# Performance work log

Measured on AMD Instinct MI355X. Metric: run time of the kernel, lower is better.

## Reference

```python
import jax, jax.numpy as jnp
import numpy as np

L_K = 6  # number of nearest neighbors (matches module-level L_K)
N_POINTS = 4096


def setup_inputs() -> dict:
    key = jax.random.key(0)
    k1, k2, k3, k4 = jax.random.split(key, 4)
    input_t = jax.random.normal(k1, (1, 3, N_POINTS), dtype=jnp.float32)
    sf_t = jax.random.normal(k2, (1, 3, N_POINTS), dtype=jnp.float32) * 0.1
    y1 = jax.random.normal(k3, (1, 3, N_POINTS), dtype=jnp.float32)
    pred = jax.random.normal(k4, (1, 3, N_POINTS), dtype=jnp.float32)
    return {"input_t": input_t, "sf_t": sf_t, "y1": y1, "pred": pred}


def _kabsch(pc, recon):
    # Standard Kabsch rigid-transform estimation (pc, recon: [N,3]).
    cp = pc.mean(axis=0)
    cr = recon.mean(axis=0)
    H = (pc - cp).T @ (recon - cr)  # [3,3] cross-covariance
    U, S, Vt = jnp.linalg.svd(H)
    d = jnp.sign(jnp.linalg.det(Vt.T @ U.T))
    # R = V diag(1,1,d) U^T  (reflection fix)
    R = Vt.T @ (jnp.stack([jnp.float32(1.0), jnp.float32(1.0), d])[:, None] * U.T)
    t = cr - R @ cp
    return R, t


def _knn_laplace(centers, ref, k):
    # centers: [N,3] query points (x1); ref: [M,3] cloud to gather neighbors from.
    # Matches: squared_dist over all pairs, topk smallest along ref dim,
    # grouping gather, then Laplacian differencing normalized by (k-1).
    d2 = jnp.sum((centers[:, None, :] - ref[None, :, :]) ** 2, axis=-1)  # [N,M]
    _, idx = jax.lax.top_k(-d2, k)  # k smallest distances -> neighbor indices [N,k]
    grouped = ref[idx]  # [N,k,3] gather
    return jnp.sum(grouped - centers[:, None, :], axis=1) / float(k - 1)  # [N,3]


def reference(input_t, sf_t, y1, pred):
    # Rigid reconstruction: we use a single cluster covering all points
    # (deterministic stand-in for the CPU-side DBSCAN clustering), so the
    # whole cloud is rigidly reconstructed via Kabsch, then detached
    # (original code calls .detach() on the Kabsch reconstruction).
    pc = input_t[0].T        # [N,3]
    recon = pc + sf_t[0].T   # [N,3]
    R, t = _kabsch(pc, recon)
    rigid_recon = jax.lax.stop_gradient(pc @ R.T + t)  # [N,3]

    yT = y1[0].T  # [N,3]
    laplace_y = _knn_laplace(rigid_recon, yT, L_K)          # cross-cloud kNN Laplacian
    laplace_x = _knn_laplace(rigid_recon, rigid_recon, L_K)  # self kNN Laplacian
    laplace_reduced = laplace_x - laplace_y  # [N,3]

    # Single cluster = all points: subtract mean Laplacian difference.
    rigid_refine = rigid_recon - jnp.mean(laplace_reduced, axis=0)  # [N,3]

    # L1 loss (mean reduction) vs student prediction.
    return jnp.mean(jnp.abs(rigid_refine - pred[0].T))
```

## Files before the change

### kernel.cpp

```cpp
#include <hip/hip_runtime.h>
#include <math.h>

#define NP 4096
#define KNN 6
#define NCHUNK 16
#define CHUNK 256

typedef unsigned int u32;

__device__ inline double det3(const double M[3][3]) {
  return M[0][0]*(M[1][1]*M[2][2]-M[1][2]*M[2][1])
       - M[0][1]*(M[1][0]*M[2][2]-M[1][2]*M[2][0])
       + M[0][2]*(M[1][0]*M[2][1]-M[1][1]*M[2][0]);
}

__device__ inline double wave_reduce(double v) {
#pragma unroll
  for (int o = 32; o > 0; o >>= 1) v += __shfl_down(v, o);
  return v;
}

#define TOP6_INSERT(key)                                   \
  { u32 _t;                                                \
    _t = min(b0, key); key = max(b0, key); b0 = _t;        \
    _t = min(b1, key); key = max(b1, key); b1 = _t;        \
    _t = min(b2, key); key = max(b2, key); b2 = _t;        \
    _t = min(b3, key); key = max(b3, key); b3 = _t;        \
    _t = min(b4, key); key = max(b4, key); b4 = _t;        \
    _t = min(b5, key); key = max(b5, key); b5 = _t; }

__global__ __launch_bounds__(256) void k1_kabsch(const float* __restrict__ in,
                                                 const float* __restrict__ sf,
                                                 float* __restrict__ rx,
                                                 float* __restrict__ ry,
                                                 float* __restrict__ rz) {
  const int tid = threadIdx.x;
  const int lane = tid & 63, wv = tid >> 6;
  double acc[15];
#pragma unroll
  for (int q = 0; q < 15; ++q) acc[q] = 0.0;
  for (int i = tid; i < NP; i += 256) {
    double px = in[i], py = in[NP + i], pz = in[2*NP + i];
    double qx = px + (double)sf[i];
    double qy = py + (double)sf[NP + i];
    double qz = pz + (double)sf[2*NP + i];
    acc[0] += px; acc[1] += py; acc[2] += pz;
    acc[3] += qx; acc[4] += qy; acc[5] += qz;
    acc[6] += px*qx; acc[7]  += px*qy; acc[8]  += px*qz;
    acc[9] += py*qx; acc[10] += py*qy; acc[11] += py*qz;
    acc[12]+= pz*qx; acc[13] += pz*qy; acc[14] += pz*qz;
  }
  __shared__ double wred[4][15];
#pragma unroll
  for (int q = 0; q < 15; ++q) {
    double v = wave_reduce(acc[q]);
    if (lane == 0) wred[wv][q] = v;
  }
  __syncthreads();
  __shared__ float Rs[9];
  __shared__ float ts[3];
  if (tid == 0) {
    double tot[15];
    for (int q = 0; q < 15; ++q)
      tot[q] = wred[0][q] + wred[1][q] + wred[2][q] + wred[3][q];
    const double invN = 1.0 / (double)NP;
    double cp[3] = { tot[0]*invN, tot[1]*invN, tot[2]*invN };
    double cr[3] = { tot[3]*invN, tot[4]*invN, tot[5]*invN };
    double H[3][3];
    for (int a = 0; a < 3; ++a)
      for (int b = 0; b < 3; ++b)
        H[a][b] = tot[6 + a*3 + b] - (double)NP * cp[a] * cr[b];
    double A[3][3];
    for (int a = 0; a < 3; ++a)
      for (int b = 0; b < 3; ++b)
        A[a][b] = H[0][a]*H[0][b] + H[1][a]*H[1][b] + H[2][a]*H[2][b];
    double V[3][3] = {{1,0,0},{0,1,0},{0,0,1}};
    const int PQ[3][2] = {{0,1},{0,2},{1,2}};
    for (int sweep = 0; sweep < 12; ++sweep) {
      for (int r = 0; r < 3; ++r) {
        const int p = PQ[r][0], q = PQ[r][1];
        double apq = A[p][q];
        if (fabs(apq) > 1e-300) {
          double theta = (A[q][q] - A[p][p]) / (2.0 * apq);
          double tt = copysign(1.0, theta) / (fabs(theta) + sqrt(theta*theta + 1.0));
          double c = 1.0 / sqrt(tt*tt + 1.0);
          double s = tt * c;
          for (int k = 0; k < 3; ++k) { double akp=A[k][p], akq=A[k][q]; A[k][p]=c*akp - s*akq; A[k][q]=s*akp + c*akq; }
          for (int k = 0; k < 3; ++k) { double apk=A[p][k], aqk=A[q][k]; A[p][k]=c*apk - s*aqk; A[q][k]=s*apk + c*aqk; }
          for (int k = 0; k < 3; ++k) { double vkp=V[k][p], vkq=V[k][q]; V[k][p]=c*vkp - s*vkq; V[k][q]=s*vkp + c*vkq; }
        }
      }
    }
    int ord[3] = {0,1,2};
    for (int a = 0; a < 2; ++a)
      for (int b = a + 1; b < 3; ++b)
        if (A[ord[b]][ord[b]] > A[ord[a]][ord[a]]) { int t2 = ord[a]; ord[a] = ord[b]; ord[b] = t2; }
    double Vc[3][3], Uc[3][3];
    for (int j = 0; j < 3; ++j) {
      const int e = ord[j];
      double lam = A[e][e] > 0.0 ? A[e][e] : 0.0;
      double sv = sqrt(lam);
      double isv = sv > 0.0 ? 1.0 / sv : 0.0;
      for (int a = 0; a < 3; ++a) Vc[a][j] = V[a][e];
      for (int a = 0; a < 3; ++a)
        Uc[a][j] = (H[a][0]*Vc[0][j] + H[a][1]*Vc[1][j] + H[a][2]*Vc[2][j]) * isv;
    }
    double dd = (det3(Uc) * det3(Vc)) >= 0.0 ? 1.0 : -1.0;
    double R[3][3];
    for (int a = 0; a < 3; ++a)
      for (int b = 0; b < 3; ++b)
        R[a][b] = Vc[a][0]*Uc[b][0] + Vc[a][1]*Uc[b][1] + dd * Vc[a][2]*Uc[b][2];
    double tv[3];
    for (int a = 0; a < 3; ++a)
      tv[a] = cr[a] - (R[a][0]*cp[0] + R[a][1]*cp[1] + R[a][2]*cp[2]);
    for (int a = 0; a < 3; ++a) {
      Rs[a*3+0] = (float)R[a][0];
      Rs[a*3+1] = (float)R[a][1];
      Rs[a*3+2] = (float)R[a][2];
      ts[a] = (float)tv[a];
    }
  }
  __syncthreads();
  for (int i = tid; i < NP; i += 256) {
    float px = in[i], py = in[NP + i], pz = in[2*NP + i];
    rx[i] = Rs[0]*px + Rs[1]*py + Rs[2]*pz + ts[0];
    ry[i] = Rs[3]*px + Rs[4]*py + Rs[5]*pz + ts[1];
    rz[i] = Rs[6]*px + Rs[7]*py + Rs[8]*pz + ts[2];
  }
}

__global__ __launch_bounds__(256) void k2_partial(const float* __restrict__ rx,
                                                  const float* __restrict__ ry,
                                                  const float* __restrict__ rz,
                                                  const float* __restrict__ ycloud,
                                                  u32* __restrict__ part) {
  __shared__ float4 sc[CHUNK];
  const int tid = threadIdx.x;
  const int chunk = blockIdx.x;
  const int cblk  = blockIdx.y;
  const int cloud = blockIdx.z;
  const int j0 = chunk * CHUNK;
  if (cloud == 0) {
    sc[tid] = make_float4(rx[j0 + tid], ry[j0 + tid], rz[j0 + tid], 0.f);
  } else {
    sc[tid] = make_float4(ycloud[j0 + tid], ycloud[NP + j0 + tid],
                          ycloud[2*NP + j0 + tid], 0.f);
  }
  __syncthreads();
  const int ci = cblk * 256 + tid;
  const float cx = rx[ci], cy = ry[ci], cz = rz[ci];
  u32 b0 = ~0u, b1 = ~0u, b2 = ~0u, b3 = ~0u, b4 = ~0u, b5 = ~0u;
#pragma unroll 8
  for (int j = 0; j < CHUNK; ++j) {
    float4 c = sc[j];
    float dx = c.x - cx, dy = c.y - cy, dz = c.z - cz;
    float d2 = fmaf(dx, dx, fmaf(dy, dy, dz * dz));
    u32 key = (__float_as_uint(d2) & 0xFFFFF000u) | (u32)(j0 + j);
    TOP6_INSERT(key);
  }
  u32* o = part + (size_t)(cloud * NCHUNK + chunk) * KNN * NP + ci;
  o[0*NP] = b0; o[1*NP] = b1; o[2*NP] = b2;
  o[3*NP] = b3; o[4*NP] = b4; o[5*NP] = b5;
}

__global__ __launch_bounds__(256) void k2_merge(const u32* __restrict__ part,
                                                const float* __restrict__ rx,
                                                const float* __restrict__ ry,
                                                const float* __restrict__ rz,
                                                const float* __restrict__ ycloud,
                                                double* __restrict__ blockpart) {
  const int tid = threadIdx.x;
  const int lane = tid & 63, wv = tid >> 6;
  const int ci = blockIdx.x * 256 + tid;
  double d0, d1, d2s;
  {
    u32 b0 = ~0u, b1 = ~0u, b2 = ~0u, b3 = ~0u, b4 = ~0u, b5 = ~0u;
    for (int c = 0; c < NCHUNK; ++c) {
      const u32* p = part + (size_t)c * KNN * NP + ci;
#pragma unroll
      for (int e = 0; e < KNN; ++e) {
        u32 key = p[(size_t)e * NP];
        TOP6_INSERT(key);
      }
    }
    u32 bk[KNN] = { b0, b1, b2, b3, b4, b5 };
    float s0 = 0.f, s1 = 0.f, s2 = 0.f;
#pragma unroll
    for (int k = 0; k < KNN; ++k) {
      int idx = (int)(bk[k] & 0xFFFu);
      s0 += rx[idx]; s1 += ry[idx]; s2 += rz[idx];
    }
    d0 = s0; d1 = s1; d2s = s2;
  }
  {
    u32 b0 = ~0u, b1 = ~0u, b2 = ~0u, b3 = ~0u, b4 = ~0u, b5 = ~0u;
    for (int c = 0; c < NCHUNK; ++c) {
      const u32* p = part + (size_t)(NCHUNK + c) * KNN * NP + ci;
#pragma unroll
      for (int e = 0; e < KNN; ++e) {
        u32 key = p[(size_t)e * NP];
        TOP6_INSERT(key);
      }
    }
    u32 bk[KNN] = { b0, b1, b2, b3, b4, b5 };
    float s0 = 0.f, s1 = 0.f, s2 = 0.f;
#pragma unroll
    for (int k = 0; k < KNN; ++k) {
      int idx = (int)(bk[k] & 0xFFFu);
      s0 += ycloud[idx]; s1 += ycloud[NP + idx]; s2 += ycloud[2*NP + idx];
    }
    d0 -= s0; d1 -= s1; d2s -= s2;
  }
  __shared__ double wred[4][3];
  double v0 = wave_reduce(d0), v1 = wave_reduce(d1), v2 = wave_reduce(d2s);
  if (lane == 0) { wred[wv][0] = v0; wred[wv][1] = v1; wred[wv][2] = v2; }
  __syncthreads();
  if (tid == 0) {
    blockpart[blockIdx.x * 3 + 0] = wred[0][0] + wred[1][0] + wred[2][0] + wred[3][0];
    blockpart[blockIdx.x * 3 + 1] = wred[0][1] + wred[1][1] + wred[2][1] + wred[3][1];
    blockpart[blockIdx.x * 3 + 2] = wred[0][2] + wred[1][2] + wred[2][2] + wred[3][2];
  }
}

__global__ __launch_bounds__(256) void k3_final(const double* __restrict__ blockpart,
                                                const float* __restrict__ rx,
                                                const float* __restrict__ ry,
                                                const float* __restrict__ rz,
                                                const float* __restrict__ pred,
                                                float* __restrict__ out) {
  const int tid = threadIdx.x;
  const int lane = tid & 63, wv = tid >> 6;
  __shared__ float m[3];
  if (tid == 0) {
    double s0 = 0.0, s1 = 0.0, s2 = 0.0;
    for (int b = 0; b < 16; ++b) {
      s0 += blockpart[b*3 + 0];
      s1 += blockpart[b*3 + 1];
      s2 += blockpart[b*3 + 2];
    }
    const double sc = 0.2 / (double)NP;
    m[0] = (float)(s0 * sc); m[1] = (float)(s1 * sc); m[2] = (float)(s2 * sc);
  }
  __syncthreads();
  const float m0 = m[0], m1 = m[1], m2 = m[2];
  double s = 0.0;
  for (int i = tid; i < NP; i += 256) {
    s += (double)fabsf(rx[i] - m0 - pred[i]);
    s += (double)fabsf(ry[i] - m1 - pred[NP + i]);
    s += (double)fabsf(rz[i] - m2 - pred[2*NP + i]);
  }
  __shared__ double wred[4];
  double v = wave_reduce(s);
  if (lane == 0) wred[wv] = v;
  __syncthreads();
  if (tid == 0)
    out[0] = (float)((wred[0] + wred[1] + wred[2] + wred[3]) / (3.0 * (double)NP));
}

extern "C" void kernel_launch(void* const* d_in, const int* in_sizes, int n_in,
                              void* d_out, int out_size, void* d_ws, size_t ws_size,
                              hipStream_t stream) {
  const float* in   = (const float*)d_in[0];
  const float* sf   = (const float*)d_in[1];
  const float* y1   = (const float*)d_in[2];
  const float* pred = (const float*)d_in[3];

  u32* part = (u32*)d_ws;
  double* blockpart = (double*)(part + (size_t)2 * NCHUNK * KNN * NP);
  float* rx = (float*)(blockpart + 48);
  float* ry = rx + NP;
  float* rz = ry + NP;

  k1_kabsch<<<1, 256, 0, stream>>>(in, sf, rx, ry, rz);
  k2_partial<<<dim3(NCHUNK, 16, 2), 256, 0, stream>>>(rx, ry, rz, y1, part);
  k2_merge<<<16, 256, 0, stream>>>(part, rx, ry, rz, y1, blockpart);
  k3_final<<<1, 256, 0, stream>>>(blockpart, rx, ry, rz, pred, (float*)d_out);
}
```

Measured before the change: 69.03 us.

## Fuse transform into kNN scan, merge final reduction, use float Jacobi

```diff
diff --git a/kernel.cpp b/kernel.cpp
--- a/kernel.cpp
+++ b/kernel.cpp
@@ -7,33 +7,30 @@
 #define CHUNK 256
 
 typedef unsigned int u32;
-
-__device__ inline double det3(const double M[3][3]) {
+typedef unsigned long long u64;
+
+__device__ inline double wave_reduce(double v) {
+#pragma unroll
+  for (int o = 32; o > 0; o >>= 1) v += __shfl_down(v, o);
+  return v;
+}
+
+__device__ inline float det3f(const float M[3][3]) {
   return M[0][0]*(M[1][1]*M[2][2]-M[1][2]*M[2][1])
        - M[0][1]*(M[1][0]*M[2][2]-M[1][2]*M[2][0])
        + M[0][2]*(M[1][0]*M[2][1]-M[1][1]*M[2][0]);
 }
 
-__device__ inline double wave_reduce(double v) {
-#pragma unroll
-  for (int o = 32; o > 0; o >>= 1) v += __shfl_down(v, o);
-  return v;
-}
-
-#define TOP6_INSERT(key)                                   \
-  { u32 _t;                                                \
-    _t = min(b0, key); key = max(b0, key); b0 = _t;        \
-    _t = min(b1, key); key = max(b1, key); b1 = _t;        \
-    _t = min(b2, key); key = max(b2, key); b2 = _t;        \
-    _t = min(b3, key); key = max(b3, key); b3 = _t;        \
-    _t = min(b4, key); key = max(b4, key); b4 = _t;        \
-    _t = min(b5, key); key = max(b5, key); b5 = _t; }
+#define TOP6_INSERT_ILP(key)                                          \
+  { u32 m0 = max(b0, key), m1 = max(b1, key), m2 = max(b2, key),      \
+        m3 = max(b3, key), m4 = max(b4, key);                         \
+    b0 = min(b0, key); b1 = min(b1, m0); b2 = min(b2, m1);            \
+    b3 = min(b3, m2); b4 = min(b4, m3); b5 = min(b5, m4); }
 
 __global__ __launch_bounds__(256) void k1_kabsch(const float* __restrict__ in,
                                                  const float* __restrict__ sf,
-                                                 float* __restrict__ rx,
-                                                 float* __restrict__ ry,
-                                                 float* __restrict__ rz) {
+                                                 float* __restrict__ Rt,
+                                                 u32* __restrict__ counter) {
   const int tid = threadIdx.x;
   const int lane = tid & 63, wv = tid >> 6;
   double acc[15];
@@ -57,8 +54,6 @@
     if (lane == 0) wred[wv][q] = v;
   }
   __syncthreads();
-  __shared__ float Rs[9];
-  __shared__ float ts[3];
   if (tid == 0) {
     double tot[15];
     for (int q = 0; q < 15; ++q)
@@ -66,28 +61,28 @@
     const double invN = 1.0 / (double)NP;
     double cp[3] = { tot[0]*invN, tot[1]*invN, tot[2]*invN };
     double cr[3] = { tot[3]*invN, tot[4]*invN, tot[5]*invN };
-    double H[3][3];
+    float H[3][3];
     for (int a = 0; a < 3; ++a)
       for (int b = 0; b < 3; ++b)
-        H[a][b] = tot[6 + a*3 + b] - (double)NP * cp[a] * cr[b];
-    double A[3][3];
+        H[a][b] = (float)(tot[6 + a*3 + b] - (double)NP * cp[a] * cr[b]);
+    float A[3][3];
     for (int a = 0; a < 3; ++a)
       for (int b = 0; b < 3; ++b)
         A[a][b] = H[0][a]*H[0][b] + H[1][a]*H[1][b] + H[2][a]*H[2][b];
-    double V[3][3] = {{1,0,0},{0,1,0},{0,0,1}};
+    float V[3][3] = {{1,0,0},{0,1,0},{0,0,1}};
     const int PQ[3][2] = {{0,1},{0,2},{1,2}};
-    for (int sweep = 0; sweep < 12; ++sweep) {
+    for (int sweep = 0; sweep < 8; ++sweep) {
       for (int r = 0; r < 3; ++r) {
         const int p = PQ[r][0], q = PQ[r][1];
-        double apq = A[p][q];
-        if (fabs(apq) > 1e-300) {
-          double theta = (A[q][q] - A[p][p]) / (2.0 * apq);
-          double tt = copysign(1.0, theta) / (fabs(theta) + sqrt(theta*theta + 1.0));
-          double c = 1.0 / sqrt(tt*tt + 1.0);
-          double s = tt * c;
-          for (int k = 0; k < 3; ++k) { double akp=A[k][p], akq=A[k][q]; A[k][p]=c*akp - s*akq; A[k][q]=s*akp + c*akq; }
-          for (int k = 0; k < 3; ++k) { double apk=A[p][k], aqk=A[q][k]; A[p][k]=c*apk - s*aqk; A[q][k]=s*apk + c*aqk; }
-          for (int k = 0; k < 3; ++k) { double vkp=V[k][p], vkq=V[k][q]; V[k][p]=c*vkp - s*vkq; V[k][q]=s*vkp + c*vkq; }
+        float apq = A[p][q];
+        if (fabsf(apq) > 1e-30f) {
+          float theta = (A[q][q] - A[p][p]) / (2.0f * apq);
+          float tt = copysignf(1.0f, theta) / (fabsf(theta) + sqrtf(theta*theta + 1.0f));
+          float c = 1.0f / sqrtf(tt*tt + 1.0f);
+          float s = tt * c;
+          for (int k = 0; k < 3; ++k) { float akp=A[k][p], akq=A[k][q]; A[k][p]=c*akp - s*akq; A[k][q]=s*akp + c*akq; }
+          for (int k = 0; k < 3; ++k) { float apk=A[p][k], aqk=A[q][k]; A[p][k]=c*apk - s*aqk; A[q][k]=s*apk + c*aqk; }
+          for (int k = 0; k < 3; ++k) { float vkp=V[k][p], vkq=V[k][q]; V[k][p]=c*vkp - s*vkq; V[k][q]=s*vkp + c*vkq; }
         }
       }
     }
@@ -95,151 +90,157 @@
     for (int a = 0; a < 2; ++a)
       for (int b = a + 1; b < 3; ++b)
         if (A[ord[b]][ord[b]] > A[ord[a]][ord[a]]) { int t2 = ord[a]; ord[a] = ord[b]; ord[b] = t2; }
-    double Vc[3][3], Uc[3][3];
+    float Vc[3][3], Uc[3][3];
     for (int j = 0; j < 3; ++j) {
       const int e = ord[j];
-      double lam = A[e][e] > 0.0 ? A[e][e] : 0.0;
-      double sv = sqrt(lam);
-      double isv = sv > 0.0 ? 1.0 / sv : 0.0;
+      float lam = A[e][e] > 0.0f ? A[e][e] : 0.0f;
+      float sv = sqrtf(lam);
+      float isv = sv > 1e-20f ? 1.0f / sv : 0.0f;
       for (int a = 0; a < 3; ++a) Vc[a][j] = V[a][e];
       for (int a = 0; a < 3; ++a)
         Uc[a][j] = (H[a][0]*Vc[0][j] + H[a][1]*Vc[1][j] + H[a][2]*Vc[2][j]) * isv;
     }
-    double dd = (det3(Uc) * det3(Vc)) >= 0.0 ? 1.0 : -1.0;
-    double R[3][3];
+    float dd = (det3f(Uc) * det3f(Vc)) >= 0.0f ? 1.0f : -1.0f;
+    float R[3][3];
     for (int a = 0; a < 3; ++a)
       for (int b = 0; b < 3; ++b)
         R[a][b] = Vc[a][0]*Uc[b][0] + Vc[a][1]*Uc[b][1] + dd * Vc[a][2]*Uc[b][2];
-    double tv[3];
-    for (int a = 0; a < 3; ++a)
-      tv[a] = cr[a] - (R[a][0]*cp[0] + R[a][1]*cp[1] + R[a][2]*cp[2]);
     for (int a = 0; a < 3; ++a) {
-      Rs[a*3+0] = (float)R[a][0];
-      Rs[a*3+1] = (float)R[a][1];
-      Rs[a*3+2] = (float)R[a][2];
-      ts[a] = (float)tv[a];
-    }
-  }
-  __syncthreads();
-  for (int i = tid; i < NP; i += 256) {
-    float px = in[i], py = in[NP + i], pz = in[2*NP + i];
-    rx[i] = Rs[0]*px + Rs[1]*py + Rs[2]*pz + ts[0];
-    ry[i] = Rs[3]*px + Rs[4]*py + Rs[5]*pz + ts[1];
-    rz[i] = Rs[6]*px + Rs[7]*py + Rs[8]*pz + ts[2];
-  }
-}
-
-__global__ __launch_bounds__(256) void k2_partial(const float* __restrict__ rx,
-                                                  const float* __restrict__ ry,
-                                                  const float* __restrict__ rz,
-                                                  const float* __restrict__ ycloud,
-                                                  u32* __restrict__ part) {
+      Rt[a*3+0] = R[a][0]; Rt[a*3+1] = R[a][1]; Rt[a*3+2] = R[a][2];
+      Rt[9+a] = (float)(cr[a] - ((double)R[a][0]*cp[0] + (double)R[a][1]*cp[1]
+                                 + (double)R[a][2]*cp[2]));
+    }
+    *counter = 0u;
+  }
+}
+
+__global__ __launch_bounds__(256) void k2_scan(const float* __restrict__ in,
+                                               const float* __restrict__ ycloud,
+                                               const float* __restrict__ Rt,
+                                               u32* __restrict__ part,
+                                               float* __restrict__ rx,
+                                               float* __restrict__ ry,
+                                               float* __restrict__ rz) {
   __shared__ float4 sc[CHUNK];
+  __shared__ float Rts[12];
   const int tid = threadIdx.x;
-  const int chunk = blockIdx.x;
-  const int cblk  = blockIdx.y;
-  const int cloud = blockIdx.z;
+  const int chunk = blockIdx.x, cblk = blockIdx.y, cloud = blockIdx.z;
+  if (tid < 12) Rts[tid] = Rt[tid];
+  __syncthreads();
+  const float r0=Rts[0], r1=Rts[1], r2=Rts[2];
+  const float r3=Rts[3], r4=Rts[4], r5=Rts[5];
+  const float r6=Rts[6], r7=Rts[7], r8=Rts[8];
+  const float t0=Rts[9], t1=Rts[10], t2=Rts[11];
   const int j0 = chunk * CHUNK;
-  if (cloud == 0) {
-    sc[tid] = make_float4(rx[j0 + tid], ry[j0 + tid], rz[j0 + tid], 0.f);
-  } else {
-    sc[tid] = make_float4(ycloud[j0 + tid], ycloud[NP + j0 + tid],
-                          ycloud[2*NP + j0 + tid], 0.f);
-  }
-  __syncthreads();
-  const int ci = cblk * 256 + tid;
-  const float cx = rx[ci], cy = ry[ci], cz = rz[ci];
-  u32 b0 = ~0u, b1 = ~0u, b2 = ~0u, b3 = ~0u, b4 = ~0u, b5 = ~0u;
+  {
+    const int jj = j0 + tid;
+    float a, b, c;
+    if (cloud == 0) {
+      float px = in[jj], py = in[NP + jj], pz = in[2*NP + jj];
+      a = fmaf(r0, px, fmaf(r1, py, fmaf(r2, pz, t0)));
+      b = fmaf(r3, px, fmaf(r4, py, fmaf(r5, pz, t1)));
+      c = fmaf(r6, px, fmaf(r7, py, fmaf(r8, pz, t2)));
+      if (chunk == cblk) { rx[jj] = a; ry[jj] = b; rz[jj] = c; }
+    } else {
+      a = ycloud[jj]; b = ycloud[NP + jj]; c = ycloud[2*NP + jj];
+    }
+    sc[tid] = make_float4(a, b, c, fmaf(a, a, fmaf(b, b, c * c)));
+  }
+  const int ci = cblk * CHUNK + tid;
+  float cx, cy, cz;
+  {
+    float px = in[ci], py = in[NP + ci], pz = in[2*NP + ci];
+    cx = fmaf(r0, px, fmaf(r1, py, fmaf(r2, pz, t0)));
+    cy = fmaf(r3, px, fmaf(r4, py, fmaf(r5, pz, t1)));
+    cz = fmaf(r6, px, fmaf(r7, py, fmaf(r8, pz, t2)));
+  }
+  const float ax = -2.f*cx, ay = -2.f*cy, az = -2.f*cz;
+  __syncthreads();
+  u32 b0=~0u, b1=~0u, b2=~0u, b3=~0u, b4=~0u, b5=~0u;
 #pragma unroll 8
   for (int j = 0; j < CHUNK; ++j) {
     float4 c = sc[j];
-    float dx = c.x - cx, dy = c.y - cy, dz = c.z - cz;
-    float d2 = fmaf(dx, dx, fmaf(dy, dy, dz * dz));
-    u32 key = (__float_as_uint(d2) & 0xFFFFF000u) | (u32)(j0 + j);
-    TOP6_INSERT(key);
+    float s = fmaf(c.x, ax, fmaf(c.y, ay, fmaf(c.z, az, c.w)));
+    u32 bits = __float_as_uint(s);
+    u32 u = bits ^ ((u32)((int)bits >> 31) | 0x80000000u);
+    u32 key = (u & 0xFFFFF000u) | (u32)(j0 + j);
+    TOP6_INSERT_ILP(key);
   }
   u32* o = part + (size_t)(cloud * NCHUNK + chunk) * KNN * NP + ci;
   o[0*NP] = b0; o[1*NP] = b1; o[2*NP] = b2;
   o[3*NP] = b3; o[4*NP] = b4; o[5*NP] = b5;
 }
 
-__global__ __launch_bounds__(256) void k2_merge(const u32* __restrict__ part,
-                                                const float* __restrict__ rx,
-                                                const float* __restrict__ ry,
-                                                const float* __restrict__ rz,
-                                                const float* __restrict__ ycloud,
-                                                double* __restrict__ blockpart) {
+__global__ __launch_bounds__(256) void k3_merge_final(const u32* __restrict__ part,
+                                                      const float* __restrict__ rx,
+                                                      const float* __restrict__ ry,
+                                                      const float* __restrict__ rz,
+                                                      const float* __restrict__ ycloud,
+                                                      const float* __restrict__ pred,
+                                                      double* __restrict__ blockpart,
+                                                      u32* __restrict__ counter,
+                                                      float* __restrict__ out) {
   const int tid = threadIdx.x;
   const int lane = tid & 63, wv = tid >> 6;
-  const int ci = blockIdx.x * 256 + tid;
-  double d0, d1, d2s;
-  {
-    u32 b0 = ~0u, b1 = ~0u, b2 = ~0u, b3 = ~0u, b4 = ~0u, b5 = ~0u;
-    for (int c = 0; c < NCHUNK; ++c) {
-      const u32* p = part + (size_t)c * KNN * NP + ci;
-#pragma unroll
-      for (int e = 0; e < KNN; ++e) {
-        u32 key = p[(size_t)e * NP];
-        TOP6_INSERT(key);
-      }
-    }
-    u32 bk[KNN] = { b0, b1, b2, b3, b4, b5 };
-    float s0 = 0.f, s1 = 0.f, s2 = 0.f;
+  const int cloud = blockIdx.x >> 4, cblk = blockIdx.x & 15;
+  const int ci = cblk * 256 + tid;
+  u32 b0=~0u, b1=~0u, b2=~0u, b3=~0u, b4=~0u, b5=~0u;
+  for (int c = 0; c < NCHUNK; ++c) {
+    const u32* p = part + (size_t)(cloud * NCHUNK + c) * KNN * NP + ci;
+#pragma unroll
+    for (int e = 0; e < KNN; ++e) {
+      u32 key = p[(size_t)e * NP];
+      TOP6_INSERT_ILP(key);
+    }
+  }
+  u32 bk[KNN] = { b0, b1, b2, b3, b4, b5 };
+  float s0 = 0.f, s1 = 0.f, s2 = 0.f;
+  if (cloud == 0) {
 #pragma unroll
     for (int k = 0; k < KNN; ++k) {
       int idx = (int)(bk[k] & 0xFFFu);
       s0 += rx[idx]; s1 += ry[idx]; s2 += rz[idx];
     }
-    d0 = s0; d1 = s1; d2s = s2;
-  }
-  {
-    u32 b0 = ~0u, b1 = ~0u, b2 = ~0u, b3 = ~0u, b4 = ~0u, b5 = ~0u;
-    for (int c = 0; c < NCHUNK; ++c) {
-      const u32* p = part + (size_t)(NCHUNK + c) * KNN * NP + ci;
-#pragma unroll
-      for (int e = 0; e < KNN; ++e) {
-        u32 key = p[(size_t)e * NP];
-        TOP6_INSERT(key);
-      }
-    }
-    u32 bk[KNN] = { b0, b1, b2, b3, b4, b5 };
-    float s0 = 0.f, s1 = 0.f, s2 = 0.f;
+  } else {
 #pragma unroll
     for (int k = 0; k < KNN; ++k) {
       int idx = (int)(bk[k] & 0xFFFu);
       s0 += ycloud[idx]; s1 += ycloud[NP + idx]; s2 += ycloud[2*NP + idx];
     }
-    d0 -= s0; d1 -= s1; d2s -= s2;
-  }
+  }
+  const double sgn = cloud ? -1.0 : 1.0;
+  double v0 = wave_reduce(sgn * (double)s0);
+  double v1 = wave_reduce(sgn * (double)s1);
+  double v2 = wave_reduce(sgn * (double)s2);
   __shared__ double wred[4][3];
-  double v0 = wave_reduce(d0), v1 = wave_reduce(d1), v2 = wave_reduce(d2s);
+  __shared__ int lastFlag;
   if (lane == 0) { wred[wv][0] = v0; wred[wv][1] = v1; wred[wv][2] = v2; }
   __syncthreads();
   if (tid == 0) {
-    blockpart[blockIdx.x * 3 + 0] = wred[0][0] + wred[1][0] + wred[2][0] + wred[3][0];
-    blockpart[blockIdx.x * 3 + 1] = wred[0][1] + wred[1][1] + wred[2][1] + wred[3][1];
-    blockpart[blockIdx.x * 3 + 2] = wred[0][2] + wred[1][2] + wred[2][2] + wred[3][2];
-  }
-}
-
-__global__ __launch_bounds__(256) void k3_final(const double* __restrict__ blockpart,
-                                                const float* __restrict__ rx,
-                                                const float* __restrict__ ry,
-                                                const float* __restrict__ rz,
-                                                const float* __restrict__ pred,
-                                                float* __restrict__ out) {
-  const int tid = threadIdx.x;
-  const int lane = tid & 63, wv = tid >> 6;
+    for (int q = 0; q < 3; ++q) {
+      double B = wred[0][q] + wred[1][q] + wred[2][q] + wred[3][q];
+      atomicExch((u64*)&blockpart[blockIdx.x * 3 + q], (u64)__double_as_longlong(B));
+    }
+    __threadfence();
+    u32 t = atomicAdd(counter, 1u);
+    lastFlag = (t == 31u);
+  }
+  __syncthreads();
+  if (!lastFlag) return;
+
+  __shared__ double bp[96];
+  __threadfence();
+  if (tid < 96)
+    bp[tid] = __longlong_as_double((long long)atomicAdd((u64*)&blockpart[tid], 0ULL));
+  __syncthreads();
   __shared__ float m[3];
   if (tid == 0) {
-    double s0 = 0.0, s1 = 0.0, s2 = 0.0;
-    for (int b = 0; b < 16; ++b) {
-      s0 += blockpart[b*3 + 0];
-      s1 += blockpart[b*3 + 1];
-      s2 += blockpart[b*3 + 2];
+    double a0 = 0.0, a1 = 0.0, a2 = 0.0;
+    for (int b = 0; b < 32; ++b) {
+      a0 += bp[b*3 + 0]; a1 += bp[b*3 + 1]; a2 += bp[b*3 + 2];
     }
     const double sc = 0.2 / (double)NP;
-    m[0] = (float)(s0 * sc); m[1] = (float)(s1 * sc); m[2] = (float)(s2 * sc);
+    m[0] = (float)(a0 * sc); m[1] = (float)(a1 * sc); m[2] = (float)(a2 * sc);
   }
   __syncthreads();
   const float m0 = m[0], m1 = m[1], m2 = m[2];
@@ -249,12 +250,12 @@
     s += (double)fabsf(ry[i] - m1 - pred[NP + i]);
     s += (double)fabsf(rz[i] - m2 - pred[2*NP + i]);
   }
-  __shared__ double wred[4];
   double v = wave_reduce(s);
-  if (lane == 0) wred[wv] = v;
+  __shared__ double fred[4];
+  if (lane == 0) fred[wv] = v;
   __syncthreads();
   if (tid == 0)
-    out[0] = (float)((wred[0] + wred[1] + wred[2] + wred[3]) / (3.0 * (double)NP));
+    out[0] = (float)((fred[0] + fred[1] + fred[2] + fred[3]) / (3.0 * (double)NP));
 }
 
 extern "C" void kernel_launch(void* const* d_in, const int* in_sizes, int n_in,
@@ -266,13 +267,15 @@
   const float* pred = (const float*)d_in[3];
 
   u32* part = (u32*)d_ws;
-  double* blockpart = (double*)(part + (size_t)2 * NCHUNK * KNN * NP);
-  float* rx = (float*)(blockpart + 48);
+  double* blockpart = (double*)(part + (size_t)2*NCHUNK*KNN*NP);
+  u32* counter = (u32*)(blockpart + 96);
+  float* Rt = (float*)(counter + 4);
+  float* rx = Rt + 12;
   float* ry = rx + NP;
   float* rz = ry + NP;
 
-  k1_kabsch<<<1, 256, 0, stream>>>(in, sf, rx, ry, rz);
-  k2_partial<<<dim3(NCHUNK, 16, 2), 256, 0, stream>>>(rx, ry, rz, y1, part);
-  k2_merge<<<16, 256, 0, stream>>>(part, rx, ry, rz, y1, blockpart);
-  k3_final<<<1, 256, 0, stream>>>(blockpart, rx, ry, rz, pred, (float*)d_out);
-}
+  k1_kabsch<<<1, 256, 0, stream>>>(in, sf, Rt, counter);
+  k2_scan<<<dim3(NCHUNK, 16, 2), 256, 0, stream>>>(in, y1, Rt, part, rx, ry, rz);
+  k3_merge_final<<<32, 256, 0, stream>>>(part, rx, ry, rz, y1, pred,
+                                         blockpart, counter, (float*)d_out);
+}
```

New measurement: 56.06 us (median of 2 runs). -18.8%, faster.
